# Optimization experiments

Measured on AMD Instinct MI355X. Metric: run time of the kernel, lower is better.

The kernel has to match this reference:

```python
import jax, jax.numpy as jnp
import numpy as np

B, TX, TS = 64, 2048, 10
D, L, NMELS, MAXR, R = 256, 1024, 80, 20, 2


def gru_cell(x, h, wih, whh, bih, bhh):
    # torch GRUCell: gates ordered (r, z, n)
    gi = x @ wih.T + bih
    gh = h @ whh.T + bhh
    ir, iz, inn = jnp.split(gi, 3, axis=-1)
    hr, hz, hn = jnp.split(gh, 3, axis=-1)
    r = jax.nn.sigmoid(ir + hr)
    z = jax.nn.sigmoid(iz + hz)
    n = jnp.tanh(inn + r * hn)
    return (1.0 - z) * n + z * h


def lstm_cell(x, h, c, wih, whh, bih, bhh):
    # torch LSTMCell: gates ordered (i, f, g, o)
    g = x @ wih.T + bih + h @ whh.T + bhh
    i, f, gg, o = jnp.split(g, 4, axis=-1)
    c_new = jax.nn.sigmoid(f) * c + jax.nn.sigmoid(i) * jnp.tanh(gg)
    h_new = jax.nn.sigmoid(o) * jnp.tanh(c_new)
    return h_new, c_new


def attention(enc, query, W, v):
    # u = v @ tanh(enc + W q); softmax over time
    qp = query @ W.T                                  # [B, D]
    u = jnp.tanh(enc + qp[:, None, :]) @ v            # [B, T]
    scores = jax.nn.softmax(u, axis=-1)               # [B, T]
    ctx = jnp.einsum('bt,btd->bd', scores, enc)       # [B, D]
    return scores, ctx


def setup_inputs() -> dict:
    key = jax.random.key(0)
    ks = jax.random.split(key, 40)
    n = lambda i, shape, s=0.02: jax.random.normal(ks[i], shape, dtype=jnp.float32) * s
    return {
        'encoder_seq': n(0, (B, TX, D), 1.0),
        'style_embed': n(1, (B, TS, D), 1.0),
        'prenet_in': n(2, (B, NMELS), 1.0),
        'h_text': n(3, (B, D), 1.0), 'h_style': n(4, (B, D), 1.0), 'h_attn': n(5, (B, D), 1.0),
        'h_r1': n(6, (B, L), 1.0), 'h_r2': n(7, (B, L), 1.0),
        'c_r1': n(8, (B, L), 1.0), 'c_r2': n(9, (B, L), 1.0),
        'cv_text': n(10, (B, D), 1.0), 'cv_style': n(11, (B, D), 1.0), 'cv': n(12, (B, D), 1.0),
        'fc1_w': n(13, (256, NMELS)), 'fc1_b': jnp.zeros((256,), jnp.float32),
        'fc2_w': n(14, (128, 256)), 'fc2_b': jnp.zeros((128,), jnp.float32),
        'tW': n(15, (D, D)), 'tv': n(16, (D,)),
        'sW': n(17, (D, D)), 'sv': n(18, (D,)),
        't_wih': n(19, (3 * D, D + 128)), 't_whh': n(20, (3 * D, D)),
        't_bih': jnp.zeros((3 * D,), jnp.float32), 't_bhh': jnp.zeros((3 * D,), jnp.float32),
        's_wih': n(21, (3 * D, D + 128)), 's_whh': n(22, (3 * D, D)),
        's_bih': jnp.zeros((3 * D,), jnp.float32), 's_bhh': jnp.zeros((3 * D,), jnp.float32),
        'a_wih': n(23, (3 * D, D + 128)), 'a_whh': n(24, (3 * D, D)),
        'a_bih': jnp.zeros((3 * D,), jnp.float32), 'a_bhh': jnp.zeros((3 * D,), jnp.float32),
        'ri_w': n(25, (L, 2 * D)), 'ri_b': jnp.zeros((L,), jnp.float32),
        'l1_wih': n(26, (4 * L, L)), 'l1_whh': n(27, (4 * L, L)),
        'l1_bih': jnp.zeros((4 * L,), jnp.float32), 'l1_bhh': jnp.zeros((4 * L,), jnp.float32),
        'l2_wih': n(28, (4 * L, L)), 'l2_whh': n(29, (4 * L, L)),
        'l2_bih': jnp.zeros((4 * L,), jnp.float32), 'l2_bhh': jnp.zeros((4 * L,), jnp.float32),
        'mp_w': n(30, (NMELS * MAXR, L)),
        't': 0,
    }


def reference(encoder_seq, style_embed, prenet_in, h_text, h_style, h_attn,
              h_r1, h_r2, c_r1, c_r2, cv_text, cv_style, cv,
              fc1_w, fc1_b, fc2_w, fc2_b, tW, tv, sW, sv,
              t_wih, t_whh, t_bih, t_bhh, s_wih, s_whh, s_bih, s_bhh,
              a_wih, a_whh, a_bih, a_bhh, ri_w, ri_b,
              l1_wih, l1_whh, l1_bih, l1_bhh, l2_wih, l2_whh, l2_bih, l2_bhh,
              mp_w, t):
    # PreNet (eval mode: no dropout)
    p = jax.nn.relu(prenet_in @ fc1_w.T + fc1_b)
    p = jax.nn.relu(p @ fc2_w.T + fc2_b)                      # [B, 128]

    text_in = jnp.concatenate([cv_text, p], axis=-1)          # [B, D+128]
    style_in = jnp.concatenate([cv_style, p], axis=-1)
    attn_in = jnp.concatenate([cv, p], axis=-1)

    h_text = gru_cell(text_in, h_text, t_wih, t_whh, t_bih, t_bhh)
    text_scores, cv_text = attention(encoder_seq, h_text, tW, tv)

    h_style = gru_cell(style_in, h_style, s_wih, s_whh, s_bih, s_bhh)
    style_scores, cv_style = attention(style_embed, h_style, sW, sv)

    cv_new = cv_text                                          # context_vec = text_context_vec
    h_attn = gru_cell(attn_in, h_attn, a_wih, a_whh, a_bih, a_bhh)

    x = jnp.concatenate([cv_new, h_attn], axis=1) @ ri_w.T + ri_b  # [B, L]
    h_r1, c_r1 = lstm_cell(x, h_r1, c_r1, l1_wih, l1_whh, l1_bih, l1_bhh)
    x = x + h_r1
    h_r2, c_r2 = lstm_cell(x, h_r2, c_r2, l2_wih, l2_whh, l2_bih, l2_bhh)
    x = x + h_r2

    mels = (x @ mp_w.T).reshape(B, NMELS, MAXR)[:, :, :R]     # [B, n_mels, r]
    return mels
```

## Files before the change

### kernel.cpp

```cpp
#include <hip/hip_runtime.h>
#include <hip/hip_bf16.h>

typedef unsigned short u16;
typedef unsigned int   u32;
typedef __attribute__((ext_vector_type(8))) short bf16x8;
typedef __attribute__((ext_vector_type(4))) float f32x4;

#define NB   64
#define NTX  2048
#define ND   256
#define NL   1024

__device__ __forceinline__ u16 f2bf(float f){
  union { float f; u32 u; } c; c.f = f;
  return (u16)((c.u + 0x7fffu + ((c.u >> 16) & 1u)) >> 16);
}
__device__ __forceinline__ u32 pk2(float a, float b){
  return (u32)f2bf(a) | ((u32)f2bf(b) << 16);
}
__device__ __forceinline__ float sigmf(float x){ return 1.f/(1.f+__expf(-x)); }
__device__ __forceinline__ float tanhf_fast(float x){
  x = fminf(fmaxf(x, -15.f), 15.f);
  float e = __expf(2.f*x);
  return (e - 1.f) / (e + 1.f);
}
__device__ __forceinline__ float dot_rowf(const float* __restrict__ row,
                                          const float* __restrict__ x, int K4){
  float acc = 0.f;
  for (int j = 0; j < K4; ++j){
    float4 w = *(const float4*)(row + j*4);
    const float* xp = x + j*4;
    acc += w.x*xp[0] + w.y*xp[1] + w.z*xp[2] + w.w*xp[3];
  }
  return acc;
}

__global__ __launch_bounds__(256) void k_pre1(
    const float* __restrict__ cv_text, const float* __restrict__ cv,
    const float* __restrict__ h_text,  const float* __restrict__ h_attn,
    const float* __restrict__ prenet_in,
    const float* __restrict__ fc1_w, const float* __restrict__ fc1_b,
    const float* __restrict__ h_r1, const float* __restrict__ h_r2,
    float* __restrict__ xtext, float* __restrict__ xattn,
    float* __restrict__ htT,  float* __restrict__ haT,
    float* __restrict__ p1T,
    u16* __restrict__ hb1, u16* __restrict__ hb2)
{
  __shared__ float ld[64][65];
  const int blk = blockIdx.x, tid = threadIdx.x;
  if (blk < 16){
    int a = blk >> 2; int c0 = (blk & 3)*64;
    const float* src = (a==0)?cv_text:(a==1)?cv:(a==2)?h_text:h_attn;
    float* dst = (a==0)?xtext:(a==1)?xattn:(a==2)?htT:haT;
    const int r = tid >> 2, q = tid & 3;
    #pragma unroll
    for (int i = 0; i < 4; ++i){
      float4 v = *(const float4*)(src + (size_t)r*256 + c0 + q*16 + i*4);
      ld[r][q*16+i*4+0] = v.x; ld[r][q*16+i*4+1] = v.y;
      ld[r][q*16+i*4+2] = v.z; ld[r][q*16+i*4+3] = v.w;
    }
    __syncthreads();
    const int cc = tid >> 2;
    #pragma unroll
    for (int i = 0; i < 4; ++i){
      int b0 = q*16 + i*4;
      float4 o = { ld[b0+0][cc], ld[b0+1][cc], ld[b0+2][cc], ld[b0+3][cc] };
      *(float4*)(dst + (size_t)(c0+cc)*64 + b0) = o;
    }
  } else if (blk < 80){
    const int wave = tid >> 6, lane = tid & 63;
    const int n = (blk - 16)*4 + wave;
    float acc = fc1_b[n];
    const float* wr = fc1_w + (size_t)n*80;
    const float* xr = prenet_in + (size_t)lane*80;
    #pragma unroll
    for (int k = 0; k < 80; k += 4){
      float4 w = *(const float4*)(wr + k);
      acc += w.x*xr[k] + w.y*xr[k+1] + w.z*xr[k+2] + w.w*xr[k+3];
    }
    p1T[n*64 + lane] = fmaxf(acc, 0.f);
  } else {
    const int t2 = blk - 80;
    const float* src = (t2 < 32) ? h_r1 : h_r2;
    u16* dst = (t2 < 32) ? hb1 : hb2;
    const int base = (t2 & 31)*2048 + tid*8;
    float4 a = *(const float4*)(src + base);
    float4 b = *(const float4*)(src + base + 4);
    uint4 o = { pk2(a.x,a.y), pk2(a.z,a.w), pk2(b.x,b.y), pk2(b.z,b.w) };
    *(uint4*)(dst + base) = o;
  }
}

__global__ __launch_bounds__(256) void k_pre2(
    const float* __restrict__ p1T,
    const float* __restrict__ fc2_w, const float* __restrict__ fc2_b,
    float* __restrict__ xtext, float* __restrict__ xattn)
{
  const int tid = threadIdx.x, w = tid >> 6, lane = tid & 63;
  const int n = blockIdx.x;
  __shared__ float red[4][64];
  float acc = 0.f;
  const float* wr = fc2_w + (size_t)n*256 + w*64;
  const float* xb = p1T + w*64*64 + lane;
  #pragma unroll
  for (int k = 0; k < 64; k += 4){
    float4 wv = *(const float4*)(wr + k);
    acc += wv.x*xb[(k+0)*64] + wv.y*xb[(k+1)*64]
         + wv.z*xb[(k+2)*64] + wv.w*xb[(k+3)*64];
  }
  red[w][lane] = acc;
  __syncthreads();
  if (w == 0){
    float v = fmaxf(red[0][lane]+red[1][lane]+red[2][lane]+red[3][lane] + fc2_b[n], 0.f);
    xtext[(size_t)(256+n)*64 + lane] = v;
    xattn[(size_t)(256+n)*64 + lane] = v;
  }
}

__global__ __launch_bounds__(256) void k_gru(
    const float* __restrict__ t_wih, const float* __restrict__ t_whh,
    const float* __restrict__ t_bih, const float* __restrict__ t_bhh,
    const float* __restrict__ a_wih, const float* __restrict__ a_whh,
    const float* __restrict__ a_bih, const float* __restrict__ a_bhh,
    const float* __restrict__ xtext, const float* __restrict__ xattn,
    const float* __restrict__ htT,  const float* __restrict__ haT,
    float* __restrict__ htnT, u16* __restrict__ xrib)
{
  const int tid = threadIdx.x, w = tid >> 6, lane = tid & 63;
  const int isA = blockIdx.x >= 256;
  const int d = blockIdx.x & 255;
  const float* wih = isA ? a_wih : t_wih;
  const float* whh = isA ? a_whh : t_whh;
  const float* xT  = isA ? xattn : xtext;
  const float* hT  = isA ? haT   : htT;
  __shared__ float red[4][6][64];
  float s0=0.f,s1=0.f,s2=0.f,s3=0.f,s4=0.f,s5=0.f;
  {
    const float* wr = wih + (size_t)d*384       + w*96;
    const float* wz = wih + (size_t)(256+d)*384 + w*96;
    const float* wn = wih + (size_t)(512+d)*384 + w*96;
    const float* xb = xT + w*96*64 + lane;
    #pragma unroll 4
    for (int k = 0; k < 96; k += 4){
      float4 ar = *(const float4*)(wr + k);
      float4 az = *(const float4*)(wz + k);
      float4 an = *(const float4*)(wn + k);
      float x0 = xb[(k+0)*64], x1 = xb[(k+1)*64];
      float x2 = xb[(k+2)*64], x3 = xb[(k+3)*64];
      s0 += ar.x*x0 + ar.y*x1 + ar.z*x2 + ar.w*x3;
      s1 += az.x*x0 + az.y*x1 + az.z*x2 + az.w*x3;
      s2 += an.x*x0 + an.y*x1 + an.z*x2 + an.w*x3;
    }
  }
  {
    const float* vr = whh + (size_t)d*256       + w*64;
    const float* vz = whh + (size_t)(256+d)*256 + w*64;
    const float* vn = whh + (size_t)(512+d)*256 + w*64;
    const float* hb = hT + w*64*64 + lane;
    #pragma unroll 4
    for (int k = 0; k < 64; k += 4){
      float4 ar = *(const float4*)(vr + k);
      float4 az = *(const float4*)(vz + k);
      float4 an = *(const float4*)(vn + k);
      float h0 = hb[(k+0)*64], h1 = hb[(k+1)*64];
      float h2 = hb[(k+2)*64], h3 = hb[(k+3)*64];
      s3 += ar.x*h0 + ar.y*h1 + ar.z*h2 + ar.w*h3;
      s4 += az.x*h0 + az.y*h1 + az.z*h2 + az.w*h3;
      s5 += an.x*h0 + an.y*h1 + an.z*h2 + an.w*h3;
    }
  }
  red[w][0][lane]=s0; red[w][1][lane]=s1; red[w][2][lane]=s2;
  red[w][3][lane]=s3; red[w][4][lane]=s4; red[w][5][lane]=s5;
  __syncthreads();
  if (w == 0){
    const float* bih = isA ? a_bih : t_bih;
    const float* bhh = isA ? a_bhh : t_bhh;
    float gir = bih[d]     + red[0][0][lane]+red[1][0][lane]+red[2][0][lane]+red[3][0][lane];
    float giz = bih[256+d] + red[0][1][lane]+red[1][1][lane]+red[2][1][lane]+red[3][1][lane];
    float gin = bih[512+d] + red[0][2][lane]+red[1][2][lane]+red[2][2][lane]+red[3][2][lane];
    float ghr = bhh[d]     + red[0][3][lane]+red[1][3][lane]+red[2][3][lane]+red[3][3][lane];
    float ghz = bhh[256+d] + red[0][4][lane]+red[1][4][lane]+red[2][4][lane]+red[3][4][lane];
    float ghn = bhh[512+d] + red[0][5][lane]+red[1][5][lane]+red[2][5][lane]+red[3][5][lane];
    float hd = hT[d*64 + lane];
    float r  = sigmf(gir + ghr), z = sigmf(giz + ghz);
    float nn = tanhf_fast(gin + r*ghn);
    float hnew = (1.f - z)*nn + z*hd;
    if (isA) xrib[(size_t)lane*512 + 256 + d] = f2bf(hnew);
    else     htnT[(size_t)d*64 + lane]        = hnew;
  }
}

__global__ __launch_bounds__(256) void k_qp(
    const float* __restrict__ tWm, const float* __restrict__ htnT,
    float* __restrict__ qp)
{
  const int tid = threadIdx.x, w = tid >> 6, lane = tid & 63;
  const int d = blockIdx.x;
  __shared__ float red[4][64];
  float acc = 0.f;
  const float* wr = tWm + (size_t)d*256 + w*64;
  const float* xb = htnT + w*64*64 + lane;
  #pragma unroll
  for (int k = 0; k < 64; k += 4){
    float4 wv = *(const float4*)(wr + k);
    acc += wv.x*xb[(k+0)*64] + wv.y*xb[(k+1)*64]
         + wv.z*xb[(k+2)*64] + wv.w*xb[(k+3)*64];
  }
  red[w][lane] = acc;
  __syncthreads();
  if (w == 0)
    qp[lane*ND + d] = red[0][lane]+red[1][lane]+red[2][lane]+red[3][lane];
}

__global__ __launch_bounds__(256) void k_attn_part(
    const float* __restrict__ enc, const float* __restrict__ qp,
    const float* __restrict__ tv,  float* __restrict__ attnP)
{
  const int tid = threadIdx.x, b = blockIdx.x, ch = blockIdx.y;
  const int wave = tid >> 6, lane = tid & 63;
  __shared__ float qpL[256], vL[256], ctxL[4][256], sL[4];
  qpL[tid] = qp[b*ND + tid];
  vL[tid]  = tv[tid];
  __syncthreads();

  const float q0 = qpL[lane*4+0], q1 = qpL[lane*4+1], q2 = qpL[lane*4+2], q3 = qpL[lane*4+3];
  const float v0 = vL[lane*4+0],  v1 = vL[lane*4+1],  v2 = vL[lane*4+2],  v3 = vL[lane*4+3];
  float cx0=0.f, cx1=0.f, cx2=0.f, cx3=0.f, sacc=0.f;
  const float* base = enc + ((size_t)b*NTX + (size_t)ch*128 + wave*32)*ND + lane*4;
  #pragma unroll 4
  for (int i = 0; i < 32; ++i){
    float4 ev = *(const float4*)(base + (size_t)i*ND);
    float e0 = ev.x, e1 = ev.y, e2 = ev.z, e3 = ev.w;
    float pp = v0*tanhf_fast(e0+q0) + v1*tanhf_fast(e1+q1)
             + v2*tanhf_fast(e2+q2) + v3*tanhf_fast(e3+q3);
    #pragma unroll
    for (int off = 1; off < 64; off <<= 1) pp += __shfl_xor(pp, off);
    float w = __expf(pp);
    sacc += w; cx0 += w*e0; cx1 += w*e1; cx2 += w*e2; cx3 += w*e3;
  }
  ctxL[wave][lane*4+0]=cx0; ctxL[wave][lane*4+1]=cx1;
  ctxL[wave][lane*4+2]=cx2; ctxL[wave][lane*4+3]=cx3;
  if (lane == 0) sL[wave] = sacc;
  __syncthreads();
  float c = ctxL[0][tid]+ctxL[1][tid]+ctxL[2][tid]+ctxL[3][tid];
  float* dst = attnP + ((size_t)b*16 + ch)*257;
  dst[tid] = c;
  if (tid == 0) dst[256] = sL[0]+sL[1]+sL[2]+sL[3];
}

__global__ __launch_bounds__(256) void k_attn_red(
    const float* __restrict__ attnP, u16* __restrict__ xrib)
{
  const int tid = threadIdx.x, b = blockIdx.x;
  float c = 0.f, s = 0.f;
  for (int ch = 0; ch < 16; ++ch){
    const float* src = attnP + ((size_t)b*16 + ch)*257;
    c += src[tid]; s += src[256];
  }
  xrib[(size_t)b*512 + tid] = f2bf(c / s);
}


__global__ __launch_bounds__(256) void k_mm_ri(
    const u16* __restrict__ xrib, const float* __restrict__ ri_w,
    const float* __restrict__ ri_b, float* __restrict__ x0,
    u16* __restrict__ x0b)
{
  __shared__ float Rs[4][4][64][4];
  const int tid = threadIdx.x, lane = tid & 63, w = tid >> 6;
  const int n0 = blockIdx.x * 16;
  f32x4 acc[4];
  #pragma unroll
  for (int i = 0; i < 4; ++i) acc[i] = (f32x4){0.f,0.f,0.f,0.f};
  const int nrow = n0 + (lane & 15);
  const float* wr = ri_w + (size_t)nrow*512 + w*128 + (lane >> 4)*8;
  const u16* xs = xrib + (size_t)(lane & 15)*512 + w*128 + (lane >> 4)*8;
  #pragma unroll
  for (int t = 0; t < 4; ++t){
    float4 wa = *(const float4*)(wr + t*32);
    float4 wb = *(const float4*)(wr + t*32 + 4);
    union { bf16x8 v; uint4 u; } bf;
    bf.u.x = pk2(wa.x,wa.y); bf.u.y = pk2(wa.z,wa.w);
    bf.u.z = pk2(wb.x,wb.y); bf.u.w = pk2(wb.z,wb.w);
    #pragma unroll
    for (int fb = 0; fb < 4; ++fb){
      union { bf16x8 v; uint4 u; } af;
      af.u = *(const uint4*)(xs + fb*16*512 + t*32);
      acc[fb] = __builtin_amdgcn_mfma_f32_16x16x32_bf16(af.v, bf.v, acc[fb], 0, 0, 0);
    }
  }
  #pragma unroll
  for (int fb = 0; fb < 4; ++fb)
    #pragma unroll
    for (int r = 0; r < 4; ++r) Rs[w][fb][lane][r] = acc[fb][r];
  __syncthreads();
  {
    const int n = n0 + (lane & 15);
    const float bias = ri_b[n];
    #pragma unroll
    for (int r = 0; r < 4; ++r){
      float v = Rs[0][w][lane][r] + Rs[1][w][lane][r]
              + Rs[2][w][lane][r] + Rs[3][w][lane][r] + bias;
      int b = w*16 + (lane >> 4)*4 + r;
      x0[(size_t)b*1024 + n]  = v;
      x0b[(size_t)b*1024 + n] = f2bf(v);
    }
  }
}

__global__ __launch_bounds__(256) void k_mm_lstm(
    const float* __restrict__ Wih, const float* __restrict__ Whh,
    const u16* __restrict__ xb, const u16* __restrict__ hb,
    float* __restrict__ P)
{
  const int tid = threadIdx.x, lane = tid & 63, g = tid >> 6;
  const int j0 = blockIdx.x * 16, s = blockIdx.y;
  const float* W = (s < 2) ? Wih : Whh;
  const u16*   X = (s < 2) ? xb  : hb;
  const int kbase = (s & 1) * 512;
  f32x4 acc[4];
  #pragma unroll
  for (int i = 0; i < 4; ++i) acc[i] = (f32x4){0.f,0.f,0.f,0.f};
  const int nrow = g*1024 + j0 + (lane & 15);
  const float* wr = W + (size_t)nrow*1024 + kbase + (lane >> 4)*8;
  const u16*   xs = X + (size_t)(lane & 15)*1024 + kbase + (lane >> 4)*8;
  #pragma unroll 4
  for (int t = 0; t < 16; ++t){
    float4 wa = *(const float4*)(wr + t*32);
    float4 wb = *(const float4*)(wr + t*32 + 4);
    union { bf16x8 v; uint4 u; } bf;
    bf.u.x = pk2(wa.x,wa.y); bf.u.y = pk2(wa.z,wa.w);
    bf.u.z = pk2(wb.x,wb.y); bf.u.w = pk2(wb.z,wb.w);
    #pragma unroll
    for (int fb = 0; fb < 4; ++fb){
      union { bf16x8 v; uint4 u; } af;
      af.u = *(const uint4*)(xs + fb*16*1024 + t*32);
      acc[fb] = __builtin_amdgcn_mfma_f32_16x16x32_bf16(af.v, bf.v, acc[fb], 0, 0, 0);
    }
  }
  const int jc = j0 + (lane & 15);
  #pragma unroll
  for (int fb = 0; fb < 4; ++fb){
    const int b = fb*16 + (lane >> 4)*4;
    #pragma unroll
    for (int r = 0; r < 4; ++r)
      P[((size_t)(s*64 + b + r))*4096 + g*1024 + jc] = acc[fb][r];
  }
}

__global__ __launch_bounds__(256) void k_cell2(
    const float* __restrict__ P,
    const float* __restrict__ bih, const float* __restrict__ bhh,
    const float* __restrict__ c_in,
    const float* __restrict__ xin, float* __restrict__ xout,
    u16* __restrict__ xoutb)
{
  const int idx = blockIdx.x*256 + threadIdx.x;
  const int b = idx >> 10, j = idx & 1023;
  float g[4];
  #pragma unroll
  for (int gg = 0; gg < 4; ++gg){
    float a = bih[gg*1024 + j] + bhh[gg*1024 + j];
    #pragma unroll
    for (int s = 0; s < 4; ++s)
      a += P[((size_t)(s*64 + b))*4096 + gg*1024 + j];
    g[gg] = a;
  }
  float ii = sigmf(g[0]), ff = sigmf(g[1]);
  float gv = tanhf_fast(g[2]), oo = sigmf(g[3]);
  float cc = ff * c_in[idx] + ii * gv;
  float hh = oo * tanhf_fast(cc);
  float xo = xin[idx] + hh;
  xout[idx]  = xo;
  xoutb[idx] = f2bf(xo);
}

__global__ __launch_bounds__(256) void k_mels(
    const float* __restrict__ x2, const float* __restrict__ mp_w,
    float* __restrict__ out)
{
  const int tid = threadIdx.x, b = blockIdx.x;
  __shared__ float xL[NL];
  #pragma unroll
  for (int i = 0; i < 4; ++i){
    int j = tid + 256*i;
    xL[j] = x2[(size_t)b*NL + j];
  }
  __syncthreads();
  if (tid < 160){
    int m = tid >> 1, r = tid & 1;
    float acc = dot_rowf(mp_w + (size_t)(m*20 + r)*NL, xL, 256);
    out[b*160 + tid] = acc;
  }
}

extern "C" void kernel_launch(void* const* d_in, const int* in_sizes, int n_in,
                              void* d_out, int out_size, void* d_ws, size_t ws_size,
                              hipStream_t stream)
{
  (void)in_sizes; (void)n_in; (void)out_size; (void)ws_size;
  const float* enc     = (const float*)d_in[0];
  const float* pre_in  = (const float*)d_in[2];
  const float* h_text  = (const float*)d_in[3];
  const float* h_attn  = (const float*)d_in[5];
  const float* h_r1    = (const float*)d_in[6];
  const float* h_r2    = (const float*)d_in[7];
  const float* c_r1    = (const float*)d_in[8];
  const float* c_r2    = (const float*)d_in[9];
  const float* cv_text = (const float*)d_in[10];
  const float* cv      = (const float*)d_in[12];
  const float* fc1_w   = (const float*)d_in[13];
  const float* fc1_b   = (const float*)d_in[14];
  const float* fc2_w   = (const float*)d_in[15];
  const float* fc2_b   = (const float*)d_in[16];
  const float* tWm     = (const float*)d_in[17];
  const float* tv      = (const float*)d_in[18];
  const float* t_wih   = (const float*)d_in[21];
  const float* t_whh   = (const float*)d_in[22];
  const float* t_bih   = (const float*)d_in[23];
  const float* t_bhh   = (const float*)d_in[24];
  const float* a_wih   = (const float*)d_in[29];
  const float* a_whh   = (const float*)d_in[30];
  const float* a_bih   = (const float*)d_in[31];
  const float* a_bhh   = (const float*)d_in[32];
  const float* ri_w    = (const float*)d_in[33];
  const float* ri_b    = (const float*)d_in[34];
  const float* l1_wih  = (const float*)d_in[35];
  const float* l1_whh  = (const float*)d_in[36];
  const float* l1_bih  = (const float*)d_in[37];
  const float* l1_bhh  = (const float*)d_in[38];
  const float* l2_wih  = (const float*)d_in[39];
  const float* l2_whh  = (const float*)d_in[40];
  const float* l2_bih  = (const float*)d_in[41];
  const float* l2_bhh  = (const float*)d_in[42];
  const float* mp_w    = (const float*)d_in[43];

  float* ws    = (float*)d_ws;
  float* qp    = ws;
  float* attnP = qp    + 16384;
  float* x0    = attnP + 263168;
  float* x1    = x0    + 65536;
  float* x2    = x1    + 65536;
  float* P     = x2    + 65536;
  float* xtext = P     + 1048576;
  float* xattn = xtext + 24576;
  float* htT   = xattn + 24576;
  float* haT   = htT   + 16384;
  float* htnT  = haT   + 16384;
  float* p1T   = htnT  + 16384;
  u16*   hb1   = (u16*)(p1T + 16384);
  u16*   hb2   = hb1 + 65536;
  u16*   xrib  = hb2 + 65536;
  u16*   x0b   = xrib + 32768;
  u16*   x1b   = x0b + 65536;
  u16*   x2b   = x1b + 65536;

  k_pre1<<<144, 256, 0, stream>>>(cv_text, cv, h_text, h_attn,
      pre_in, fc1_w, fc1_b, h_r1, h_r2,
      xtext, xattn, htT, haT, p1T, hb1, hb2);
  k_pre2<<<128, 256, 0, stream>>>(p1T, fc2_w, fc2_b, xtext, xattn);
  k_gru<<<512, 256, 0, stream>>>(t_wih, t_whh, t_bih, t_bhh,
      a_wih, a_whh, a_bih, a_bhh, xtext, xattn, htT, haT, htnT, xrib);
  k_qp<<<256, 256, 0, stream>>>(tWm, htnT, qp);

  k_attn_part<<<dim3(64,16), 256, 0, stream>>>(enc, qp, tv, attnP);
  k_attn_red<<<64, 256, 0, stream>>>(attnP, xrib);

  k_mm_ri<<<64, 256, 0, stream>>>(xrib, ri_w, ri_b, x0, x0b);

  k_mm_lstm<<<dim3(64,4), 256, 0, stream>>>(l1_wih, l1_whh, x0b, hb1, P);
  k_cell2<<<256, 256, 0, stream>>>(P, l1_bih, l1_bhh, c_r1, x0, x1, x1b);

  k_mm_lstm<<<dim3(64,4), 256, 0, stream>>>(l2_wih, l2_whh, x1b, hb2, P);
  k_cell2<<<256, 256, 0, stream>>>(P, l2_bih, l2_bhh, c_r2, x1, x2, x2b);

  k_mels<<<64, 256, 0, stream>>>(x2, mp_w, (float*)d_out);
}
```

Before: 120.2 us.

## Fuse LSTM gate matmul with cell update via in-block split-K reduction

Merges the LSTM matmul kernel and the elementwise cell kernel into one kernel. Each block now covers 4 hidden units across all 4 gates, and its four waves each compute one K-split (x/h halves). The partials are reduced in shared memory and the LSTM cell is applied directly, which removes the 4MB partial-sum buffer round trip and one launch per layer. The cost is that each wave re-reads the activation tiles for fewer output columns, and reads of the weight rows become strided across gates.

```diff
diff --git a/kernel.cpp b/kernel.cpp
--- a/kernel.cpp
+++ b/kernel.cpp
@@ -308,22 +308,28 @@
   }
 }
 
-__global__ __launch_bounds__(256) void k_mm_lstm(
+__global__ __launch_bounds__(256) void k_lstm(
     const float* __restrict__ Wih, const float* __restrict__ Whh,
     const u16* __restrict__ xb, const u16* __restrict__ hb,
-    float* __restrict__ P)
-{
-  const int tid = threadIdx.x, lane = tid & 63, g = tid >> 6;
-  const int j0 = blockIdx.x * 16, s = blockIdx.y;
-  const float* W = (s < 2) ? Wih : Whh;
-  const u16*   X = (s < 2) ? xb  : hb;
-  const int kbase = (s & 1) * 512;
+    const float* __restrict__ bih, const float* __restrict__ bhh,
+    const float* __restrict__ c_in,
+    const float* __restrict__ xin, float* __restrict__ xout,
+    u16* __restrict__ xoutb)
+{
+  __shared__ float Rs[4][4][64][4];
+  const int tid = threadIdx.x, lane = tid & 63, w = tid >> 6;
+  const int j0 = blockIdx.x * 4;
+  const float* W = (w < 2) ? Wih : Whh;
+  const u16*   X = (w < 2) ? xb  : hb;
+  const int kbase = (w & 1) * 512;
+
   f32x4 acc[4];
   #pragma unroll
   for (int i = 0; i < 4; ++i) acc[i] = (f32x4){0.f,0.f,0.f,0.f};
-  const int nrow = g*1024 + j0 + (lane & 15);
-  const float* wr = W + (size_t)nrow*1024 + kbase + (lane >> 4)*8;
-  const u16*   xs = X + (size_t)(lane & 15)*1024 + kbase + (lane >> 4)*8;
+  const int r16 = lane & 15;
+  const int g = r16 >> 2, jq = r16 & 3;
+  const float* wr = W + (size_t)(g*1024 + j0 + jq)*1024 + kbase + (lane >> 4)*8;
+  const u16*   xs = X + (size_t)r16*1024 + kbase + (lane >> 4)*8;
   #pragma unroll 4
   for (int t = 0; t < 16; ++t){
     float4 wa = *(const float4*)(wr + t*32);
@@ -334,45 +340,35 @@
     #pragma unroll
     for (int fb = 0; fb < 4; ++fb){
       union { bf16x8 v; uint4 u; } af;
-      af.u = *(const uint4*)(xs + fb*16*1024 + t*32);
+      af.u = *(const uint4*)(X + (size_t)(fb*16 + r16)*1024 + kbase + (lane >> 4)*8 + t*32);
       acc[fb] = __builtin_amdgcn_mfma_f32_16x16x32_bf16(af.v, bf.v, acc[fb], 0, 0, 0);
     }
   }
-  const int jc = j0 + (lane & 15);
-  #pragma unroll
-  for (int fb = 0; fb < 4; ++fb){
-    const int b = fb*16 + (lane >> 4)*4;
-    #pragma unroll
-    for (int r = 0; r < 4; ++r)
-      P[((size_t)(s*64 + b + r))*4096 + g*1024 + jc] = acc[fb][r];
-  }
-}
-
-__global__ __launch_bounds__(256) void k_cell2(
-    const float* __restrict__ P,
-    const float* __restrict__ bih, const float* __restrict__ bhh,
-    const float* __restrict__ c_in,
-    const float* __restrict__ xin, float* __restrict__ xout,
-    u16* __restrict__ xoutb)
-{
-  const int idx = blockIdx.x*256 + threadIdx.x;
-  const int b = idx >> 10, j = idx & 1023;
-  float g[4];
+  (void)xs;
+  #pragma unroll
+  for (int fb = 0; fb < 4; ++fb)
+    #pragma unroll
+    for (int r = 0; r < 4; ++r) Rs[w][fb][lane][r] = acc[fb][r];
+  __syncthreads();
+
+  const int b  = tid >> 2, jq2 = tid & 3;
+  const int j  = j0 + jq2;
+  const int fb = b >> 4, q = (b >> 2) & 3, reg = b & 3;
+  float gate[4];
   #pragma unroll
   for (int gg = 0; gg < 4; ++gg){
-    float a = bih[gg*1024 + j] + bhh[gg*1024 + j];
-    #pragma unroll
-    for (int s = 0; s < 4; ++s)
-      a += P[((size_t)(s*64 + b))*4096 + gg*1024 + j];
-    g[gg] = a;
-  }
-  float ii = sigmf(g[0]), ff = sigmf(g[1]);
-  float gv = tanhf_fast(g[2]), oo = sigmf(g[3]);
-  float cc = ff * c_in[idx] + ii * gv;
+    const int li = q*16 + gg*4 + jq2;
+    gate[gg] = bih[gg*1024 + j] + bhh[gg*1024 + j]
+             + Rs[0][fb][li][reg] + Rs[1][fb][li][reg]
+             + Rs[2][fb][li][reg] + Rs[3][fb][li][reg];
+  }
+  float ii = sigmf(gate[0]), ff = sigmf(gate[1]);
+  float gv = tanhf_fast(gate[2]), oo = sigmf(gate[3]);
+  float cc = ff * c_in[(size_t)b*1024 + j] + ii * gv;
   float hh = oo * tanhf_fast(cc);
-  float xo = xin[idx] + hh;
-  xout[idx]  = xo;
-  xoutb[idx] = f2bf(xo);
+  float xo = xin[(size_t)b*1024 + j] + hh;
+  xout[(size_t)b*1024 + j]  = xo;
+  xoutb[(size_t)b*1024 + j] = f2bf(xo);
 }
 
 __global__ __launch_bounds__(256) void k_mels(
@@ -441,8 +437,7 @@
   float* x0    = attnP + 263168;
   float* x1    = x0    + 65536;
   float* x2    = x1    + 65536;
-  float* P     = x2    + 65536;
-  float* xtext = P     + 1048576;
+  float* xtext = x2    + 65536;
   float* xattn = xtext + 24576;
   float* htT   = xattn + 24576;
   float* haT   = htT   + 16384;
@@ -468,11 +463,10 @@
 
   k_mm_ri<<<64, 256, 0, stream>>>(xrib, ri_w, ri_b, x0, x0b);
 
-  k_mm_lstm<<<dim3(64,4), 256, 0, stream>>>(l1_wih, l1_whh, x0b, hb1, P);
-  k_cell2<<<256, 256, 0, stream>>>(P, l1_bih, l1_bhh, c_r1, x0, x1, x1b);
-
-  k_mm_lstm<<<dim3(64,4), 256, 0, stream>>>(l2_wih, l2_whh, x1b, hb2, P);
-  k_cell2<<<256, 256, 0, stream>>>(P, l2_bih, l2_bhh, c_r2, x1, x2, x2b);
+  k_lstm<<<256, 256, 0, stream>>>(l1_wih, l1_whh, x0b, hb1,
+      l1_bih, l1_bhh, c_r1, x0, x1, x1b);
+  k_lstm<<<256, 256, 0, stream>>>(l2_wih, l2_whh, x1b, hb2,
+      l2_bih, l2_bhh, c_r2, x1, x2, x2b);
 
   k_mels<<<64, 256, 0, stream>>>(x2, mp_w, (float*)d_out);
 }
```

Result: faster. 117.2 us (-2.5%).
